# Optimization experiments

Measured on AMD Instinct MI355X. Metric: run time of the kernel, lower is better.

The kernel has to match this reference:

```python
import jax, jax.numpy as jnp
import numpy as np
from jax import lax

C_IN, C_OUT, LEVEL = 64, 128, 4
SOFTMAX_SCALE = 10.0
ESCAPE_NAN = 1e-4


def conv3(x, w, b):
    y = lax.conv_general_dilated(x, w, (1, 1), [(1, 1), (1, 1)],
                                 dimension_numbers=('NCHW', 'OIHW', 'NCHW'))
    return y + b[None, :, None, None]


def conv1(x, w, b):  # 1x1 conv, w: [O, I]
    return jnp.einsum('oi,bihw->bohw', w, x) + b[None, :, None, None]


def prelu(x, a):
    return jnp.where(x >= 0, x, a * x)


def resblock(x, w1, b1, w2, b2):  # EDSR ResBlock, res_scale=1
    return x + conv3(jax.nn.relu(conv3(x, w1, b1)), w2, b2)


def patches9(x):
    # 3x3 'same' (zero-pad 1) patches: [B,C,H,W] -> [B,C,3,3,H*W], (C,kh,kw) order like torch unfold
    B, C, H, W = x.shape
    xp = jnp.pad(x, ((0, 0), (0, 0), (1, 1), (1, 1)))
    p = jnp.stack([xp[:, :, i:i + H, j:j + W] for i in range(3) for j in range(3)], axis=2)
    return p.reshape(B, C, 3, 3, H * W)


def pyramid_attention(x, mbw, mbb, mba, mw, mb_, ma, aw, ab, aa):
    B, C, H, W = x.shape
    C2 = C // 2
    scales = [1.0 - i / 10 for i in range(LEVEL)]
    match_base = prelu(conv1(x, mbw, mbb), mba)            # [B,C2,H,W]
    xp = patches9(match_base).reshape(B, C2 * 9, H * W)    # query patches (same-padded input to conv2d)
    w_all, rw_all = [], []
    for s in scales:
        if s != 1.0:
            Hs, Ws = int(H * s), int(W * s)
            ref = jax.image.resize(x, (B, C, Hs, Ws), method='bilinear')
        else:
            ref = x
        base = prelu(conv1(ref, aw, ab), aa)               # conv_assembly: [B,C,Hs,Ws]
        rw_all.append(jnp.transpose(patches9(base), (0, 4, 1, 2, 3)))   # [B,L,C,3,3]
        refm = prelu(conv1(ref, mw, mb_), ma)              # conv_match:    [B,C2,Hs,Ws]
        w_all.append(jnp.transpose(patches9(refm), (0, 4, 1, 2, 3)))    # [B,L,C2,3,3]
    wi = jnp.concatenate(w_all, axis=1)                    # [B,Lt,C2,3,3]
    rw = jnp.concatenate(rw_all, axis=1)                   # [B,Lt,C,3,3]
    Lt = wi.shape[1]
    norm = jnp.maximum(jnp.sqrt(jnp.sum(wi * wi, axis=(2, 3, 4), keepdims=True)), ESCAPE_NAN)
    wn = (wi / norm).reshape(B, Lt, C2 * 9)
    # conv2d-as-correlation: scores[b,l,p] = <patch_p(match_base_b), wn[b,l]>
    scores = jnp.einsum('blk,bkp->blp', wn, xp)            # [B,Lt,H*W]
    att = jax.nn.softmax(scores * SOFTMAX_SCALE, axis=1).reshape(B, Lt, H, W)

    def tconv(y, rw_b):  # conv_transpose2d(stride=1, padding=1) == conv with swapped+flipped kernel
        wk = jnp.flip(jnp.transpose(rw_b, (1, 0, 2, 3)), axis=(2, 3))  # [C,Lt,3,3]
        return lax.conv_general_dilated(y[None], wk, (1, 1), [(1, 1), (1, 1)],
                                        dimension_numbers=('NCHW', 'OIHW', 'NCHW'))[0]

    out = jax.vmap(tconv)(att, rw) / 4.0
    return out + x  # res_scale = 1


def reference(x, bb0_w, bb0_b, bb0_a, rb1_w1, rb1_b1, rb1_w2, rb1_b2,
              pamb_w, pamb_b, pamb_a, pam_w, pam_b, pam_a, paa_w, paa_b, paa_a,
              rb2_w1, rb2_b1, rb2_w2, rb2_b2):
    h = lax.reduce_window(x, -jnp.inf, lax.max, (1, 1, 2, 2), (1, 1, 2, 2), 'VALID')  # MaxPool2d(2)
    h = prelu(conv3(h, bb0_w, bb0_b), bb0_a)               # BasicBlock in->out
    h = resblock(h, rb1_w1, rb1_b1, rb1_w2, rb1_b2)
    h = pyramid_attention(h, pamb_w, pamb_b, pamb_a, pam_w, pam_b, pam_a, paa_w, paa_b, paa_a)
    h = resblock(h, rb2_w1, rb2_b1, rb2_w2, rb2_b2)
    return h


def setup_inputs() -> dict:
    key = jax.random.key(0)
    ks = jax.random.split(key, 20)
    B, H, W = 2, 128, 128
    Ci, Co = C_IN, C_OUT
    C2 = Co // 2

    def n(k, shape, s=0.05):
        return jax.random.normal(k, shape, jnp.float32) * s

    a = jnp.asarray(0.25, jnp.float32)  # PReLU default init
    return {
        'x': jax.random.normal(ks[0], (B, Ci, H, W), jnp.float32),
        'bb0_w': n(ks[1], (Co, Ci, 3, 3)), 'bb0_b': n(ks[2], (Co,)), 'bb0_a': a,
        'rb1_w1': n(ks[3], (Co, Co, 3, 3)), 'rb1_b1': n(ks[4], (Co,)),
        'rb1_w2': n(ks[5], (Co, Co, 3, 3)), 'rb1_b2': n(ks[6], (Co,)),
        'pamb_w': n(ks[7], (C2, Co)), 'pamb_b': n(ks[8], (C2,)), 'pamb_a': a,
        'pam_w': n(ks[9], (C2, Co)), 'pam_b': n(ks[10], (C2,)), 'pam_a': a,
        'paa_w': n(ks[11], (Co, Co)), 'paa_b': n(ks[12], (Co,)), 'paa_a': a,
        'rb2_w1': n(ks[13], (Co, Co, 3, 3)), 'rb2_b1': n(ks[14], (Co,)),
        'rb2_w2': n(ks[15], (Co, Co, 3, 3)), 'rb2_b2': n(ks[16], (Co,)),
    }
```

## Files before the change

### kernel.cpp

```cpp
#include <hip/hip_runtime.h>

typedef unsigned short u16;
typedef __attribute__((ext_vector_type(8))) __bf16 bf16x8;
typedef __attribute__((ext_vector_type(8))) unsigned short ushort8;
typedef __attribute__((ext_vector_type(4))) float f32x4;

__device__ __forceinline__ float bf2f(u16 u) { return __uint_as_float(((unsigned)u) << 16); }
__device__ __forceinline__ u16 f2bf(float f) {
    unsigned x = __float_as_uint(f);
    x += 0x7fffu + ((x >> 16) & 1u);
    return (u16)(x >> 16);
}

#define LP 13824

__global__ __launch_bounds__(256) void d7_gemm(
    const u16* __restrict__ A, const u16* __restrict__ B,
    int N, int K, int kLen, int mTiles, int S,
    long aBS, long bBS,
    const float* __restrict__ bias, const float* __restrict__ alpha, int act,
    const float* __restrict__ resid, long residBS,
    float* __restrict__ outF, long oFBS,
    u16* __restrict__ outB, long oBBS,
    float* __restrict__ outP, long pMN)
{
    __shared__ u16 As[128 * 40];
    __shared__ u16 Bs[128 * 40];

    const int tid = threadIdx.x;
    const int wv = tid >> 6, lane = tid & 63;
    const int wm = wv >> 1, wn = wv & 1;
    const int bn = blockIdx.x;
    const int bm = blockIdx.y % mTiles;
    const int ks = blockIdx.y / mTiles;
    const int z  = blockIdx.z;
    const int kStart = ks * kLen;

    const int srow = tid >> 1;
    const int soff = (tid & 1) * 16;
    const u16* gA = A + z * aBS + (size_t)(bm * 128 + srow) * K + kStart + soff;
    const u16* gB = B + z * bBS + (size_t)(bn * 128 + srow) * K + kStart + soff;
    u16* lA = &As[srow * 40 + soff];
    u16* lB = &Bs[srow * 40 + soff];

    f32x4 acc[4][4] = {};

    for (int k0 = 0; k0 < kLen; k0 += 32) {
        __syncthreads();
        ((uint4*)lA)[0] = ((const uint4*)gA)[0];
        ((uint4*)lA)[1] = ((const uint4*)gA)[1];
        ((uint4*)lB)[0] = ((const uint4*)gB)[0];
        ((uint4*)lB)[1] = ((const uint4*)gB)[1];
        gA += 32; gB += 32;
        __syncthreads();

        bf16x8 a[4], b[4];
        #pragma unroll
        for (int mt = 0; mt < 4; ++mt)
            a[mt] = *reinterpret_cast<const bf16x8*>(&As[(wm * 64 + mt * 16 + (lane & 15)) * 40 + (lane >> 4) * 8]);
        #pragma unroll
        for (int nt = 0; nt < 4; ++nt)
            b[nt] = *reinterpret_cast<const bf16x8*>(&Bs[(wn * 64 + nt * 16 + (lane & 15)) * 40 + (lane >> 4) * 8]);
        #pragma unroll
        for (int mt = 0; mt < 4; ++mt)
            #pragma unroll
            for (int nt = 0; nt < 4; ++nt)
                acc[mt][nt] = __builtin_amdgcn_mfma_f32_16x16x32_bf16(a[mt], b[nt], acc[mt][nt], 0, 0, 0);
    }

    if (outP) {
        float* pp = outP + ((size_t)z * S + ks) * pMN;
        #pragma unroll
        for (int mt = 0; mt < 4; ++mt) {
            const int mg = bm * 128 + wm * 64 + mt * 16 + ((lane >> 4) << 2);
            #pragma unroll
            for (int nt = 0; nt < 4; ++nt) {
                const int ng = bn * 128 + wn * 64 + nt * 16 + (lane & 15);
                #pragma unroll
                for (int r = 0; r < 4; ++r)
                    pp[(size_t)(mg + r) * N + ng] = acc[mt][nt][r];
            }
        }
        return;
    }

    const float aval = (act == 1) ? alpha[0] : 0.0f;
    #pragma unroll
    for (int mt = 0; mt < 4; ++mt) {
        const int mg = bm * 128 + wm * 64 + mt * 16 + ((lane >> 4) << 2);
        float bv[4] = {0.f, 0.f, 0.f, 0.f};
        if (bias) {
            #pragma unroll
            for (int r = 0; r < 4; ++r) bv[r] = bias[mg + r];
        }
        #pragma unroll
        for (int nt = 0; nt < 4; ++nt) {
            const int ng = bn * 128 + wn * 64 + nt * 16 + (lane & 15);
            #pragma unroll
            for (int r = 0; r < 4; ++r) {
                float t = acc[mt][nt][r] + bv[r];
                if (act == 1) t = (t >= 0.f) ? t : aval * t;
                else if (act == 2) t = fmaxf(t, 0.f);
                if (resid) t += resid[z * residBS + (size_t)(mg + r) * N + ng];
                if (outF) outF[z * oFBS + (size_t)(mg + r) * N + ng] = t;
                if (outB) outB[z * oBBS + (size_t)(mg + r) * N + ng] = f2bf(t);
            }
        }
    }
}

__global__ __launch_bounds__(256) void d7_epi(
    const float* __restrict__ parts, int S, long sStride, long bStride,
    const float* __restrict__ bias, const float* __restrict__ alpha, int act,
    const float* __restrict__ resid, long residBS, float scale,
    float* __restrict__ out, long outBS, int total)
{
    int i = blockIdx.x * 256 + threadIdx.x;
    if (i >= total) return;
    int b = blockIdx.z;
    const float* p = parts + b * bStride + i;
    float s = 0.f;
    for (int t = 0; t < S; ++t) s += p[(size_t)t * sStride];
    s *= scale;
    if (bias) s += bias[i >> 12];
    if (act == 1) { float a = alpha[0]; s = (s >= 0.f) ? s : a * s; }
    else if (act == 2) s = fmaxf(s, 0.f);
    if (resid) s += resid[b * residBS + i];
    out[b * outBS + i] = s;
}

__global__ __launch_bounds__(256) void d7_cast(const float* __restrict__ src, u16* __restrict__ dst, int n) {
    int i = blockIdx.x * 256 + threadIdx.x;
    if (i < n) dst[i] = f2bf(src[i]);
}

__global__ __launch_bounds__(256) void d7_maxpool(const float* __restrict__ x, float* __restrict__ out) {
    int p = blockIdx.x * 256 + threadIdx.x;
    int c = blockIdx.y, b = blockIdx.z;
    int oh = p >> 6, ow = p & 63;
    const float* ip = x + ((size_t)b * 64 + c) * 16384;
    float v0 = ip[(2 * oh) * 128 + 2 * ow];
    float v1 = ip[(2 * oh) * 128 + 2 * ow + 1];
    float v2 = ip[(2 * oh + 1) * 128 + 2 * ow];
    float v3 = ip[(2 * oh + 1) * 128 + 2 * ow + 1];
    out[((size_t)b * 64 + c) * 4096 + p] = fmaxf(fmaxf(v0, v1), fmaxf(v2, v3));
}

__global__ __launch_bounds__(256) void d7_im2col(const float* __restrict__ img, u16* __restrict__ patT,
                                                 int Cin, long inBS, long outBS) {
    int K = Cin * 9;
    int k = blockIdx.x * 256 + threadIdx.x;
    if (k >= K) return;
    int p = blockIdx.y, b = blockIdx.z;
    int c = k / 9, k9 = k - c * 9;
    int h = p >> 6, w = p & 63;
    int y = h + k9 / 3 - 1, x = w + (k9 % 3) - 1;
    const float* ip = img + b * inBS;
    float v = (y >= 0 && y < 64 && x >= 0 && x < 64) ? ip[(size_t)c * 4096 + y * 64 + x] : 0.f;
    patT[b * outBS + (size_t)p * K + k] = f2bf(v);
}

__global__ __launch_bounds__(256) void d7_c1T(
    const float* __restrict__ in, long inBS, const float* __restrict__ Wm,
    const float* __restrict__ bias, const float* __restrict__ alpha,
    int P, u16* __restrict__ out, long outBS, int HS, int Wp, int off)
{
    int p = blockIdx.x * 256 + threadIdx.x;
    if (p >= P) return;
    int co = blockIdx.y, b = blockIdx.z;
    const float* ip = in + b * inBS;
    float acc = bias[co];
    for (int ci = 0; ci < 128; ++ci) acc += Wm[co * 128 + ci] * ip[(size_t)ci * P + p];
    float a = alpha[0];
    acc = (acc >= 0.f) ? acc : a * acc;
    int hs = p / HS, ws = p - hs * HS;
    int lp = off + (hs + 1) * Wp + ws + 1;
    out[b * outBS + (size_t)lp * 64 + co] = f2bf(acc);
}

__global__ __launch_bounds__(256) void d7_c1N(
    const float* __restrict__ in, long inBS, const float* __restrict__ Wm,
    const float* __restrict__ bias, const float* __restrict__ alpha,
    int P, u16* __restrict__ out, long outBS, int HS, int Wp, int off)
{
    int p = blockIdx.x * 256 + threadIdx.x;
    if (p >= P) return;
    int co = blockIdx.y, b = blockIdx.z;
    const float* ip = in + b * inBS;
    float acc = bias[co];
    for (int ci = 0; ci < 128; ++ci) acc += Wm[co * 128 + ci] * ip[(size_t)ci * P + p];
    float a = alpha[0];
    acc = (acc >= 0.f) ? acc : a * acc;
    int hs = p / HS, ws = p - hs * HS;
    int lp = off + (hs + 1) * Wp + ws + 1;
    out[b * outBS + (size_t)co * LP + lp] = f2bf(acc);
}

template <int OS>
__device__ __forceinline__ void d7_taps(int o, int& i0, float w3[3]) {
    const float inv = 64.0f / OS;
    float s = (o + 0.5f) * inv - 0.5f;
    i0 = (int)ceilf(s - inv);
    float wsum = 0.f;
    #pragma unroll
    for (int t = 0; t < 3; ++t) {
        int y = i0 + t;
        float wt = 1.0f - fabsf((float)y - s) / inv;
        wt = (wt > 0.f && y >= 0 && y < 64) ? wt : 0.f;
        w3[t] = wt; wsum += wt;
    }
    float r = 1.0f / wsum;
    w3[0] *= r; w3[1] *= r; w3[2] *= r;
}

template <int OS>
__global__ __launch_bounds__(256) void d7_resize(const float* __restrict__ in, float* __restrict__ out, long out_bs) {
    int p = blockIdx.x * 256 + threadIdx.x;
    if (p >= OS * OS) return;
    int c = blockIdx.y, b = blockIdx.z;
    int oh = p / OS, ow = p - oh * OS;
    const float* img = in + ((size_t)b * 128 + c) * 4096;
    int y0, x0; float wy[3], wx[3];
    d7_taps<OS>(oh, y0, wy);
    d7_taps<OS>(ow, x0, wx);
    float sum = 0.f;
    #pragma unroll
    for (int iy = 0; iy < 3; ++iy) {
        if (wy[iy] <= 0.f) continue;
        float rs = 0.f;
        #pragma unroll
        for (int ix = 0; ix < 3; ++ix) {
            if (wx[ix] <= 0.f) continue;
            rs += wx[ix] * img[(y0 + iy) * 64 + (x0 + ix)];
        }
        sum += wy[iy] * rs;
    }
    out[(size_t)b * out_bs + (size_t)c * OS * OS + p] = sum;
}

__device__ __forceinline__ int d7_scaleW(int l) {
    return (l < 4752) ? 72 : (l < 8528) ? 64 : (l < 11496) ? 56 : 48;
}

__global__ __launch_bounds__(256) void d7_s2(const u16* __restrict__ refmT, float* __restrict__ s2) {
    int l = blockIdx.x * 256 + threadIdx.x;
    if (l >= LP) return;
    int zb = blockIdx.z;
    const u16* r = refmT + (size_t)zb * LP * 64 + (size_t)l * 64;
    float s = 0.f;
    #pragma unroll
    for (int c8 = 0; c8 < 8; ++c8) {
        ushort8 v = *reinterpret_cast<const ushort8*>(r + c8 * 8);
        #pragma unroll
        for (int i = 0; i < 8; ++i) { float f = bf2f(v[i]); s += f * f; }
    }
    s2[zb * LP + l] = s;
}

__global__ __launch_bounds__(256) void d7_rnormk(const float* __restrict__ s2, float* __restrict__ rnorm) {
    int l = blockIdx.x * 256 + threadIdx.x;
    if (l >= LP) return;
    int zb = blockIdx.z;
    int off, W, HS;
    if (l < 4752)       { off = 0;     W = 72; HS = 64; }
    else if (l < 8528)  { off = 4752;  W = 64; HS = 57; }
    else if (l < 11496) { off = 8528;  W = 56; HS = 51; }
    else                { off = 11496; W = 48; HS = 44; }
    int li = l - off, y = li / W, x = li - y * W;
    float v = 0.f;
    if (y >= 1 && y <= HS && x >= 1 && x <= HS) {
        const float* s = s2 + zb * LP;
        float a = 0.f;
        #pragma unroll
        for (int dy = -1; dy <= 1; ++dy)
            #pragma unroll
            for (int dx = -1; dx <= 1; ++dx)
                a += s[l + dy * W + dx];
        v = 1.f / fmaxf(sqrtf(a), 1e-4f);
    }
    rnorm[zb * LP + l] = v;
}

__global__ __launch_bounds__(256) void d7_st1(const u16* __restrict__ in, u16* __restrict__ out,
                                              const float* __restrict__ rnorm) {
    int vg = blockIdx.x * 256 + threadIdx.x;
    if (vg >= LP / 8) return;
    int l8 = vg << 3;
    int p = blockIdx.y;
    int h = p >> 6, w = p & 63;
    int W = d7_scaleW(l8);
    float acc[8] = {0.f, 0.f, 0.f, 0.f, 0.f, 0.f, 0.f, 0.f};
    #pragma unroll
    for (int a = -1; a <= 1; ++a) {
        int ph = h + a;
        if ((unsigned)ph >= 64u) continue;
        #pragma unroll
        for (int b = -1; b <= 1; ++b) {
            int pw = w + b;
            if ((unsigned)pw >= 64u) continue;
            const u16* rp = in + (size_t)(p + a * 64 + b) * LP + l8 + a * W;
            ushort8 v = *reinterpret_cast<const ushort8*>(rp);
            if (b == 0) {
                #pragma unroll
                for (int i = 0; i < 8; ++i) acc[i] += bf2f(v[i]);
            } else if (b == -1) {
                acc[0] += bf2f(rp[-1]);
                #pragma unroll
                for (int i = 1; i < 8; ++i) acc[i] += bf2f(v[i - 1]);
            } else {
                acc[7] += bf2f(rp[8]);
                #pragma unroll
                for (int i = 0; i < 7; ++i) acc[i] += bf2f(v[i + 1]);
            }
        }
    }
    const float4 rn0 = *reinterpret_cast<const float4*>(rnorm + l8);
    const float4 rn1 = *reinterpret_cast<const float4*>(rnorm + l8 + 4);
    float rn[8] = {rn0.x, rn0.y, rn0.z, rn0.w, rn1.x, rn1.y, rn1.z, rn1.w};
    ushort8 res;
    #pragma unroll
    for (int i = 0; i < 8; ++i)
        res[i] = f2bf((rn[i] != 0.f) ? acc[i] * rn[i] : -1e4f);
    *reinterpret_cast<ushort8*>(out + (size_t)p * LP + l8) = res;
}

__global__ __launch_bounds__(256) void d7_stats(const u16* __restrict__ sc, float2* __restrict__ stat) {
    int p = blockIdx.x, tid = threadIdx.x, wv = tid >> 6, lane = tid & 63;
    const u16* row = sc + (size_t)p * LP;
    float m = -3e38f;
    #pragma unroll
    for (int it = 0; it < 7; ++it) {
        int vg = tid + it * 256;
        if (vg < LP / 8) {
            ushort8 v = *reinterpret_cast<const ushort8*>(row + vg * 8);
            #pragma unroll
            for (int i = 0; i < 8; ++i) m = fmaxf(m, bf2f(v[i]));
        }
    }
    #pragma unroll
    for (int o = 1; o < 64; o <<= 1) m = fmaxf(m, __shfl_xor(m, o));
    __shared__ float red[4];
    if (lane == 0) red[wv] = m;
    __syncthreads();
    m = fmaxf(fmaxf(red[0], red[1]), fmaxf(red[2], red[3]));
    __syncthreads();
    float s = 0.f;
    #pragma unroll
    for (int it = 0; it < 7; ++it) {
        int vg = tid + it * 256;
        if (vg < LP / 8) {
            ushort8 v = *reinterpret_cast<const ushort8*>(row + vg * 8);
            #pragma unroll
            for (int i = 0; i < 8; ++i) s += __expf((bf2f(v[i]) - m) * 10.f);
        }
    }
    #pragma unroll
    for (int o = 1; o < 64; o <<= 1) s += __shfl_xor(s, o);
    if (lane == 0) red[wv] = s;
    __syncthreads();
    if (tid == 0) {
        float Z = red[0] + red[1] + red[2] + red[3];
        stat[p] = make_float2(m, 1.0f / Z);
    }
}

__global__ __launch_bounds__(256) void d7_st2(const u16* __restrict__ in,
                                              const float2* __restrict__ stat,
                                              const float* __restrict__ rnorm,
                                              u16* __restrict__ out) {
    int vg = blockIdx.x * 256 + threadIdx.x;
    if (vg >= LP / 8) return;
    int l8 = vg << 3;
    int p = blockIdx.y;
    int h = p >> 6, w = p & 63;
    int W = d7_scaleW(l8);
    float acc[8] = {0.f, 0.f, 0.f, 0.f, 0.f, 0.f, 0.f, 0.f};
    #pragma unroll
    for (int a = -1; a <= 1; ++a) {
        int ph = h + a;
        if ((unsigned)ph >= 64u) continue;
        #pragma unroll
        for (int b = -1; b <= 1; ++b) {
            int pw = w + b;
            if ((unsigned)pw >= 64u) continue;
            int r = p + a * 64 + b;
            float2 st = stat[r];
            const u16* rp = in + (size_t)r * LP + l8 + a * W;
            ushort8 v = *reinterpret_cast<const ushort8*>(rp);
            if (b == 0) {
                #pragma unroll
                for (int i = 0; i < 8; ++i) acc[i] += __expf((bf2f(v[i]) - st.x) * 10.f) * st.y;
            } else if (b == -1) {
                acc[0] += __expf((bf2f(rp[-1]) - st.x) * 10.f) * st.y;
                #pragma unroll
                for (int i = 1; i < 8; ++i) acc[i] += __expf((bf2f(v[i - 1]) - st.x) * 10.f) * st.y;
            } else {
                acc[7] += __expf((bf2f(rp[8]) - st.x) * 10.f) * st.y;
                #pragma unroll
                for (int i = 0; i < 7; ++i) acc[i] += __expf((bf2f(v[i + 1]) - st.x) * 10.f) * st.y;
            }
        }
    }
    const float4 rn0 = *reinterpret_cast<const float4*>(rnorm + l8);
    const float4 rn1 = *reinterpret_cast<const float4*>(rnorm + l8 + 4);
    float rn[8] = {rn0.x, rn0.y, rn0.z, rn0.w, rn1.x, rn1.y, rn1.z, rn1.w};
    ushort8 res;
    #pragma unroll
    for (int i = 0; i < 8; ++i)
        res[i] = f2bf((rn[i] != 0.f) ? acc[i] : 0.f);
    *reinterpret_cast<ushort8*>(out + (size_t)p * LP + l8) = res;
}

extern "C" void kernel_launch(void* const* d_in, const int* in_sizes, int n_in,
                              void* d_out, int out_size, void* d_ws, size_t ws_size,
                              hipStream_t stream) {
    const float* x      = (const float*)d_in[0];
    const float* bb0_w  = (const float*)d_in[1];
    const float* bb0_b  = (const float*)d_in[2];
    const float* bb0_a  = (const float*)d_in[3];
    const float* rb1_w1 = (const float*)d_in[4];
    const float* rb1_b1 = (const float*)d_in[5];
    const float* rb1_w2 = (const float*)d_in[6];
    const float* rb1_b2 = (const float*)d_in[7];
    const float* pamb_w = (const float*)d_in[8];
    const float* pamb_b = (const float*)d_in[9];
    const float* pamb_a = (const float*)d_in[10];
    const float* pam_w  = (const float*)d_in[11];
    const float* pam_b  = (const float*)d_in[12];
    const float* pam_a  = (const float*)d_in[13];
    const float* paa_w  = (const float*)d_in[14];
    const float* paa_b  = (const float*)d_in[15];
    const float* paa_a  = (const float*)d_in[16];
    const float* rb2_w1 = (const float*)d_in[17];
    const float* rb2_b1 = (const float*)d_in[18];
    const float* rb2_w2 = (const float*)d_in[19];
    const float* rb2_b2 = (const float*)d_in[20];
    float* out = (float*)d_out;
    (void)in_sizes; (void)n_in; (void)out_size; (void)ws_size;

    char* wp = (char*)d_ws;
    auto alloc = [&](size_t nbytes) { void* p = wp; wp += (nbytes + 255) & ~(size_t)255; return p; };
    const size_t BIG = 4096ull * LP * 2;
    char* big1r  = (char*)alloc(BIG + 1024);
    char* big2r  = (char*)alloc(BIG + 1024);
    float* h0f   = (float*)alloc(2ull * 64 * 4096 * 4);
    float* h1f   = (float*)alloc(2ull * 128 * 4096 * 4);
    float* h2f   = (float*)alloc(2ull * 128 * 4096 * 4);
    float* paf   = (float*)alloc(2ull * 128 * 4096 * 4);
    float* tbuf  = (float*)alloc(2ull * 128 * 4096 * 4);
    float* refb  = (float*)alloc(2ull * 128 * 7786 * 4);
    u16* mbT     = (u16*)alloc(2ull * 4096 * 64 * 2);
    u16* refmT   = (u16*)alloc(2ull * LP * 64 * 2);
    u16* baseA   = (u16*)alloc(2ull * 128 * LP * 2);
    float* s2b   = (float*)alloc(2ull * LP * 4);
    float* rnorm = (float*)alloc(2ull * LP * 4);
    float2* stat = (float2*)alloc(4096ull * 8);
    u16* A0      = (u16*)alloc(73728ull * 2);
    u16* A1      = (u16*)alloc(147456ull * 2);
    u16* A2      = (u16*)alloc(147456ull * 2);
    u16* A3      = (u16*)alloc(147456ull * 2);
    u16* A4      = (u16*)alloc(147456ull * 2);

    u16* patT    = (u16*)big1r;
    u16* S0T     = (u16*)(big1r + 512);
    u16* gT      = (u16*)(big1r + 512);
    u16* scT     = (u16*)(big2r + 512);
    float* parts = (float*)big2r;

    const long h2bs = 128L * 4096;
    const long pMN = 128L * 4096;
    const long refbs = 128L * 7786;
    const long mbTbs = 4096L * 64, rmTbs = (long)LP * 64, baBS = 128L * LP;

    auto conv = [&](const float* src, const u16* W, int Cin, const float* bias,
                    const float* alpha, int act, const float* resid, float* dst) {
        int K = Cin * 9;
        d7_im2col<<<dim3((K + 255) / 256, 4096, 2), 256, 0, stream>>>(src, patT, Cin, (long)Cin * 4096, 4096L * K);
        d7_gemm<<<dim3(32, 6, 2), 256, 0, stream>>>(W, patT, 4096, K, K / 6, 1, 6,
            0, 4096L * K, nullptr, nullptr, 0, nullptr, 0,
            nullptr, 0, nullptr, 0, parts, pMN);
        d7_epi<<<dim3(2048, 1, 2), 256, 0, stream>>>(parts, 6, pMN, 6 * pMN,
            bias, alpha, act, resid, h2bs, 1.0f, dst, h2bs, (int)pMN);
    };

    d7_cast<<<dim3(288), 256, 0, stream>>>(bb0_w, A0, 73728);
    d7_cast<<<dim3(576), 256, 0, stream>>>(rb1_w1, A1, 147456);
    d7_cast<<<dim3(576), 256, 0, stream>>>(rb1_w2, A2, 147456);
    d7_cast<<<dim3(576), 256, 0, stream>>>(rb2_w1, A3, 147456);
    d7_cast<<<dim3(576), 256, 0, stream>>>(rb2_w2, A4, 147456);

    d7_maxpool<<<dim3(16, 64, 2), 256, 0, stream>>>(x, h0f);
    conv(h0f, A0, 64, bb0_b, bb0_a, 1, nullptr, h1f);
    conv(h1f, A1, 128, rb1_b1, nullptr, 2, nullptr, tbuf);
    conv(tbuf, A2, 128, rb1_b2, nullptr, 0, h1f, h2f);

    d7_resize<57><<<dim3(13, 128, 2), 256, 0, stream>>>(h2f, refb, refbs);
    d7_resize<51><<<dim3(11, 128, 2), 256, 0, stream>>>(h2f, refb + 3249L * 128, refbs);
    d7_resize<44><<<dim3(8, 128, 2), 256, 0, stream>>>(h2f, refb + 5850L * 128, refbs);

    hipMemsetAsync(refmT, 0, 2ull * LP * 64 * 2, stream);
    hipMemsetAsync(baseA, 0, 2ull * 128 * LP * 2, stream);
    d7_c1T<<<dim3(16, 64, 2), 256, 0, stream>>>(h2f, h2bs, pamb_w, pamb_b, pamb_a, 4096, mbT, mbTbs, 64, 64, -65);
    d7_c1T<<<dim3(16, 64, 2), 256, 0, stream>>>(h2f, h2bs, pam_w, pam_b, pam_a, 4096, refmT, rmTbs, 64, 72, 0);
    d7_c1T<<<dim3(13, 64, 2), 256, 0, stream>>>(refb, refbs, pam_w, pam_b, pam_a, 3249, refmT, rmTbs, 57, 64, 4752);
    d7_c1T<<<dim3(11, 64, 2), 256, 0, stream>>>(refb + 3249L * 128, refbs, pam_w, pam_b, pam_a, 2601, refmT, rmTbs, 51, 56, 8528);
    d7_c1T<<<dim3(8, 64, 2), 256, 0, stream>>>(refb + 5850L * 128, refbs, pam_w, pam_b, pam_a, 1936, refmT, rmTbs, 44, 48, 11496);
    d7_c1N<<<dim3(16, 128, 2), 256, 0, stream>>>(h2f, h2bs, paa_w, paa_b, paa_a, 4096, baseA, baBS, 64, 72, 0);
    d7_c1N<<<dim3(13, 128, 2), 256, 0, stream>>>(refb, refbs, paa_w, paa_b, paa_a, 3249, baseA, baBS, 57, 64, 4752);
    d7_c1N<<<dim3(11, 128, 2), 256, 0, stream>>>(refb + 3249L * 128, refbs, paa_w, paa_b, paa_a, 2601, baseA, baBS, 51, 56, 8528);
    d7_c1N<<<dim3(8, 128, 2), 256, 0, stream>>>(refb + 5850L * 128, refbs, paa_w, paa_b, paa_a, 1936, baseA, baBS, 44, 48, 11496);

    d7_s2<<<dim3(54, 1, 2), 256, 0, stream>>>(refmT, s2b);
    d7_rnormk<<<dim3(54, 1, 2), 256, 0, stream>>>(s2b, rnorm);

    for (int b = 0; b < 2; ++b) {
        d7_gemm<<<dim3(LP / 128, 32, 1), 256, 0, stream>>>(mbT + b * mbTbs, refmT + b * rmTbs,
            LP, 64, 64, 32, 1, 0, 0, nullptr, nullptr, 0, nullptr, 0,
            nullptr, 0, S0T, 0, nullptr, 0);
        d7_st1<<<dim3(7, 4096), 256, 0, stream>>>(S0T, scT, rnorm + b * LP);
        d7_stats<<<dim3(4096), 256, 0, stream>>>(scT, stat);
        d7_st2<<<dim3(7, 4096), 256, 0, stream>>>(scT, stat, rnorm + b * LP, gT);
        d7_gemm<<<dim3(32, 12, 1), 256, 0, stream>>>(baseA + b * baBS, gT,
            4096, LP, LP / 12, 1, 12, 0, 0, nullptr, nullptr, 0, nullptr, 0,
            nullptr, 0, nullptr, 0, parts, pMN);
        d7_epi<<<dim3(2048, 1, 1), 256, 0, stream>>>(parts, 12, pMN, 0,
            nullptr, nullptr, 0, h2f + b * h2bs, 0, 0.25f, paf + b * h2bs, 0, (int)pMN);
    }

    conv(paf, A3, 128, rb2_b1, nullptr, 2, nullptr, tbuf);
    conv(tbuf, A4, 128, rb2_b2, nullptr, 0, paf, out);
}
```

Before: 1.087 ms.

## Move attention 1x1 convs onto MFMA GEMM and store softmax scores in fp16

The scalar 1x1 convolution kernels that built the match and assembly features are replaced by two batched bf16 MFMA GEMMs with concatenated weights and per-row PReLU. Their inputs are produced by tiled transposes, and their outputs are scattered into the padded layouts by small copy kernels. The score GEMM now emits a transposed packed store, and the softmax scale of 10 is folded into the inverse norm. Intermediate scores are kept as fp16 instead of bf16, which gives more mantissa but less range, and the extra launches plus transpose and scatter passes add memory traffic.

```diff
diff --git a/kernel.cpp b/kernel.cpp
--- a/kernel.cpp
+++ b/kernel.cpp
@@ -10,6 +10,12 @@
     unsigned x = __float_as_uint(f);
     x += 0x7fffu + ((x >> 16) & 1u);
     return (u16)(x >> 16);
+}
+__device__ __forceinline__ u16 f2h16(float f) {
+    _Float16 h = (_Float16)f; u16 r; __builtin_memcpy(&r, &h, 2); return r;
+}
+__device__ __forceinline__ float h162f(u16 u) {
+    _Float16 h; __builtin_memcpy(&h, &u, 2); return (float)h;
 }
 
 #define LP 13824
@@ -22,6 +28,7 @@
     const float* __restrict__ resid, long residBS,
     float* __restrict__ outF, long oFBS,
     u16* __restrict__ outB, long oBBS,
+    u16* __restrict__ outT, int ldT, long oTBS,
     float* __restrict__ outP, long pMN)
 {
     __shared__ u16 As[128 * 40];
@@ -84,26 +91,46 @@
         return;
     }
 
-    const float aval = (act == 1) ? alpha[0] : 0.0f;
+    const float avalS = (act == 1) ? alpha[0] : 0.0f;
     #pragma unroll
     for (int mt = 0; mt < 4; ++mt) {
         const int mg = bm * 128 + wm * 64 + mt * 16 + ((lane >> 4) << 2);
-        float bv[4] = {0.f, 0.f, 0.f, 0.f};
+        float bv[4] = {0.f, 0.f, 0.f, 0.f}, av[4];
         if (bias) {
             #pragma unroll
             for (int r = 0; r < 4; ++r) bv[r] = bias[mg + r];
+        }
+        if (act == 3) {
+            #pragma unroll
+            for (int r = 0; r < 4; ++r) av[r] = alpha[mg + r];
         }
         #pragma unroll
         for (int nt = 0; nt < 4; ++nt) {
             const int ng = bn * 128 + wn * 64 + nt * 16 + (lane & 15);
+            float v[4];
             #pragma unroll
             for (int r = 0; r < 4; ++r) {
                 float t = acc[mt][nt][r] + bv[r];
-                if (act == 1) t = (t >= 0.f) ? t : aval * t;
+                if (act == 1) t = (t >= 0.f) ? t : avalS * t;
                 else if (act == 2) t = fmaxf(t, 0.f);
+                else if (act == 3) t = (t >= 0.f) ? t : av[r] * t;
                 if (resid) t += resid[z * residBS + (size_t)(mg + r) * N + ng];
-                if (outF) outF[z * oFBS + (size_t)(mg + r) * N + ng] = t;
-                if (outB) outB[z * oBBS + (size_t)(mg + r) * N + ng] = f2bf(t);
+                v[r] = t;
+            }
+            if (outF) {
+                #pragma unroll
+                for (int r = 0; r < 4; ++r) outF[z * oFBS + (size_t)(mg + r) * N + ng] = v[r];
+            }
+            if (outB) {
+                #pragma unroll
+                for (int r = 0; r < 4; ++r) outB[z * oBBS + (size_t)(mg + r) * N + ng] = f2bf(v[r]);
+            }
+            if (outT) {
+                unsigned long long pk = (unsigned long long)f2bf(v[0])
+                    | ((unsigned long long)f2bf(v[1]) << 16)
+                    | ((unsigned long long)f2bf(v[2]) << 32)
+                    | ((unsigned long long)f2bf(v[3]) << 48);
+                *reinterpret_cast<unsigned long long*>(outT + z * oTBS + (size_t)ng * ldT + mg) = pk;
             }
         }
     }
@@ -134,6 +161,31 @@
     if (i < n) dst[i] = f2bf(src[i]);
 }
 
+__global__ __launch_bounds__(256) void d7_wbuild(
+    const float* __restrict__ pamb_w, const float* __restrict__ pam_w, const float* __restrict__ paa_w,
+    const float* __restrict__ pamb_b, const float* __restrict__ pam_b, const float* __restrict__ paa_b,
+    const float* __restrict__ pamb_a, const float* __restrict__ pam_a, const float* __restrict__ paa_a,
+    u16* __restrict__ W1, u16* __restrict__ W2,
+    float* __restrict__ b1, float* __restrict__ a1,
+    float* __restrict__ b2, float* __restrict__ a2)
+{
+    int i = blockIdx.x * 256 + threadIdx.x;
+    if (i < 256 * 128) {
+        int r = i >> 7, c = i & 127;
+        float w1 = (r < 64) ? pamb_w[r * 128 + c] : (r < 128) ? pam_w[(r - 64) * 128 + c] : paa_w[(r - 128) * 128 + c];
+        W1[i] = f2bf(w1);
+        float w2 = (r < 64) ? pam_w[r * 128 + c] : (r < 192) ? paa_w[(r - 64) * 128 + c] : 0.f;
+        W2[i] = f2bf(w2);
+    }
+    if (i < 256) {
+        int r = i;
+        b1[r] = (r < 64) ? pamb_b[r] : (r < 128) ? pam_b[r - 64] : paa_b[r - 128];
+        a1[r] = (r < 64) ? pamb_a[0] : (r < 128) ? pam_a[0] : paa_a[0];
+        b2[r] = (r < 64) ? pam_b[r] : (r < 192) ? paa_b[r - 64] : 0.f;
+        a2[r] = (r < 64) ? pam_a[0] : (r < 192) ? paa_a[0] : 0.f;
+    }
+}
+
 __global__ __launch_bounds__(256) void d7_maxpool(const float* __restrict__ x, float* __restrict__ out) {
     int p = blockIdx.x * 256 + threadIdx.x;
     int c = blockIdx.y, b = blockIdx.z;
@@ -160,40 +212,49 @@
     patT[b * outBS + (size_t)p * K + k] = f2bf(v);
 }
 
-__global__ __launch_bounds__(256) void d7_c1T(
-    const float* __restrict__ in, long inBS, const float* __restrict__ Wm,
-    const float* __restrict__ bias, const float* __restrict__ alpha,
-    int P, u16* __restrict__ out, long outBS, int HS, int Wp, int off)
-{
+__global__ __launch_bounds__(256) void d7_t32(const float* __restrict__ in, long inBS, int P,
+                                              u16* __restrict__ out, long outBS) {
+    __shared__ float tile[32][33];
+    int p0 = blockIdx.x * 32, c0 = blockIdx.y * 32, b = blockIdx.z;
+    int tx = threadIdx.x & 31, ty = threadIdx.x >> 5;
+    const float* ip = in + b * inBS;
+    #pragma unroll
+    for (int i = 0; i < 32; i += 8) {
+        int c = c0 + ty + i, p = p0 + tx;
+        tile[ty + i][tx] = (p < P) ? ip[(size_t)c * P + p] : 0.f;
+    }
+    __syncthreads();
+    u16* op = out + b * outBS;
+    #pragma unroll
+    for (int i = 0; i < 32; i += 8) {
+        int p = p0 + ty + i, c = c0 + tx;
+        if (p < P) op[(size_t)p * 128 + c] = f2bf(tile[tx][ty + i]);
+    }
+}
+
+__global__ __launch_bounds__(256) void d7_scK(const u16* __restrict__ cT, long cBS, int ldC, int colBase,
+                                              int pOff, int P, int HS, int Wp, int off,
+                                              u16* __restrict__ dst, long dBS) {
+    int t = blockIdx.x * 256 + threadIdx.x;
+    int p = t >> 3, cg = t & 7;
+    if (p >= P) return;
+    int b = blockIdx.z;
+    ushort8 v = *reinterpret_cast<const ushort8*>(cT + b * cBS + (size_t)(pOff + p) * ldC + colBase + cg * 8);
+    int h = p / HS, w = p - h * HS;
+    int lp = off + (h + 1) * Wp + w + 1;
+    *reinterpret_cast<ushort8*>(dst + b * dBS + (size_t)lp * 64 + cg * 8) = v;
+}
+
+__global__ __launch_bounds__(256) void d7_scR(const u16* __restrict__ cO, long cBS, int ldC, int rowBase,
+                                              int pOff, int P, int HS, int Wp, int off,
+                                              u16* __restrict__ dst, long dBS) {
     int p = blockIdx.x * 256 + threadIdx.x;
     if (p >= P) return;
     int co = blockIdx.y, b = blockIdx.z;
-    const float* ip = in + b * inBS;
-    float acc = bias[co];
-    for (int ci = 0; ci < 128; ++ci) acc += Wm[co * 128 + ci] * ip[(size_t)ci * P + p];
-    float a = alpha[0];
-    acc = (acc >= 0.f) ? acc : a * acc;
-    int hs = p / HS, ws = p - hs * HS;
-    int lp = off + (hs + 1) * Wp + ws + 1;
-    out[b * outBS + (size_t)lp * 64 + co] = f2bf(acc);
-}
-
-__global__ __launch_bounds__(256) void d7_c1N(
-    const float* __restrict__ in, long inBS, const float* __restrict__ Wm,
-    const float* __restrict__ bias, const float* __restrict__ alpha,
-    int P, u16* __restrict__ out, long outBS, int HS, int Wp, int off)
-{
-    int p = blockIdx.x * 256 + threadIdx.x;
-    if (p >= P) return;
-    int co = blockIdx.y, b = blockIdx.z;
-    const float* ip = in + b * inBS;
-    float acc = bias[co];
-    for (int ci = 0; ci < 128; ++ci) acc += Wm[co * 128 + ci] * ip[(size_t)ci * P + p];
-    float a = alpha[0];
-    acc = (acc >= 0.f) ? acc : a * acc;
-    int hs = p / HS, ws = p - hs * HS;
-    int lp = off + (hs + 1) * Wp + ws + 1;
-    out[b * outBS + (size_t)co * LP + lp] = f2bf(acc);
+    u16 v = cO[b * cBS + (size_t)(rowBase + co) * ldC + pOff + p];
+    int h = p / HS, w = p - h * HS;
+    int lp = off + (h + 1) * Wp + w + 1;
+    dst[b * dBS + (size_t)co * LP + lp] = v;
 }
 
 template <int OS>
@@ -276,7 +337,7 @@
             #pragma unroll
             for (int dx = -1; dx <= 1; ++dx)
                 a += s[l + dy * W + dx];
-        v = 1.f / fmaxf(sqrtf(a), 1e-4f);
+        v = 10.f / fmaxf(sqrtf(a), 1e-4f);
     }
     rnorm[zb * LP + l] = v;
 }
@@ -320,7 +381,7 @@
     ushort8 res;
     #pragma unroll
     for (int i = 0; i < 8; ++i)
-        res[i] = f2bf((rn[i] != 0.f) ? acc[i] * rn[i] : -1e4f);
+        res[i] = f2h16((rn[i] != 0.f) ? acc[i] * rn[i] : -1e4f);
     *reinterpret_cast<ushort8*>(out + (size_t)p * LP + l8) = res;
 }
 
@@ -334,7 +395,7 @@
         if (vg < LP / 8) {
             ushort8 v = *reinterpret_cast<const ushort8*>(row + vg * 8);
             #pragma unroll
-            for (int i = 0; i < 8; ++i) m = fmaxf(m, bf2f(v[i]));
+            for (int i = 0; i < 8; ++i) m = fmaxf(m, h162f(v[i]));
         }
     }
     #pragma unroll
@@ -351,7 +412,7 @@
         if (vg < LP / 8) {
             ushort8 v = *reinterpret_cast<const ushort8*>(row + vg * 8);
             #pragma unroll
-            for (int i = 0; i < 8; ++i) s += __expf((bf2f(v[i]) - m) * 10.f);
+            for (int i = 0; i < 8; ++i) s += __expf(h162f(v[i]) - m);
         }
     }
     #pragma unroll
@@ -389,15 +450,15 @@
             ushort8 v = *reinterpret_cast<const ushort8*>(rp);
             if (b == 0) {
                 #pragma unroll
-                for (int i = 0; i < 8; ++i) acc[i] += __expf((bf2f(v[i]) - st.x) * 10.f) * st.y;
+                for (int i = 0; i < 8; ++i) acc[i] += __expf(h162f(v[i]) - st.x) * st.y;
             } else if (b == -1) {
-                acc[0] += __expf((bf2f(rp[-1]) - st.x) * 10.f) * st.y;
-                #pragma unroll
-                for (int i = 1; i < 8; ++i) acc[i] += __expf((bf2f(v[i - 1]) - st.x) * 10.f) * st.y;
+                acc[0] += __expf(h162f(rp[-1]) - st.x) * st.y;
+                #pragma unroll
+                for (int i = 1; i < 8; ++i) acc[i] += __expf(h162f(v[i - 1]) - st.x) * st.y;
             } else {
-                acc[7] += __expf((bf2f(rp[8]) - st.x) * 10.f) * st.y;
-                #pragma unroll
-                for (int i = 0; i < 7; ++i) acc[i] += __expf((bf2f(v[i + 1]) - st.x) * 10.f) * st.y;
+                acc[7] += __expf(h162f(rp[8]) - st.x) * st.y;
+                #pragma unroll
+                for (int i = 0; i < 7; ++i) acc[i] += __expf(h162f(v[i + 1]) - st.x) * st.y;
             }
         }
     }
@@ -448,29 +509,43 @@
     float* h2f   = (float*)alloc(2ull * 128 * 4096 * 4);
     float* paf   = (float*)alloc(2ull * 128 * 4096 * 4);
     float* tbuf  = (float*)alloc(2ull * 128 * 4096 * 4);
-    float* refb  = (float*)alloc(2ull * 128 * 7786 * 4);
     u16* mbT     = (u16*)alloc(2ull * 4096 * 64 * 2);
     u16* refmT   = (u16*)alloc(2ull * LP * 64 * 2);
     u16* baseA   = (u16*)alloc(2ull * 128 * LP * 2);
     float* s2b   = (float*)alloc(2ull * LP * 4);
     float* rnorm = (float*)alloc(2ull * LP * 4);
     float2* stat = (float2*)alloc(4096ull * 8);
+    u16* W1      = (u16*)alloc(256ull * 128 * 2);
+    u16* W2      = (u16*)alloc(256ull * 128 * 2);
+    float* b1v   = (float*)alloc(256 * 4);
+    float* a1v   = (float*)alloc(256 * 4);
+    float* b2v   = (float*)alloc(256 * 4);
+    float* a2v   = (float*)alloc(256 * 4);
     u16* A0      = (u16*)alloc(73728ull * 2);
     u16* A1      = (u16*)alloc(147456ull * 2);
     u16* A2      = (u16*)alloc(147456ull * 2);
     u16* A3      = (u16*)alloc(147456ull * 2);
     u16* A4      = (u16*)alloc(147456ull * 2);
-
     u16* patT    = (u16*)big1r;
+    u16* h2T     = (u16*)big1r;
+    u16* refbT   = (u16*)(big1r + (4ull << 20));
     u16* S0T     = (u16*)(big1r + 512);
     u16* gT      = (u16*)(big1r + 512);
+    float* parts = (float*)big2r;
+    u16* cT1     = (u16*)big2r;
+    u16* cOut1   = (u16*)(big2r + (4ull << 20));
+    u16* cT2     = (u16*)(big2r + (8ull << 20));
+    u16* cOut2   = (u16*)(big2r + (16ull << 20));
+    float* refb  = (float*)(big2r + (26ull << 20));
     u16* scT     = (u16*)(big2r + 512);
-    float* parts = (float*)big2r;
 
     const long h2bs = 128L * 4096;
     const long pMN = 128L * 4096;
     const long refbs = 128L * 7786;
     const long mbTbs = 4096L * 64, rmTbs = (long)LP * 64, baBS = 128L * LP;
+    const long cT1bs = 4096L * 256, cO1bs = 256L * 4096;
+    const long cT2bs = 7808L * 256, cO2bs = 256L * 7808;
+    const long rbTbs = 7808L * 128;
 
     auto conv = [&](const float* src, const u16* W, int Cin, const float* bias,
                     const float* alpha, int act, const float* resid, float* dst) {
@@ -478,7 +553,7 @@
         d7_im2col<<<dim3((K + 255) / 256, 4096, 2), 256, 0, stream>>>(src, patT, Cin, (long)Cin * 4096, 4096L * K);
         d7_gemm<<<dim3(32, 6, 2), 256, 0, stream>>>(W, patT, 4096, K, K / 6, 1, 6,
             0, 4096L * K, nullptr, nullptr, 0, nullptr, 0,
-            nullptr, 0, nullptr, 0, parts, pMN);
+            nullptr, 0, nullptr, 0, nullptr, 0, 0, parts, pMN);
         d7_epi<<<dim3(2048, 1, 2), 256, 0, stream>>>(parts, 6, pMN, 6 * pMN,
             bias, alpha, act, resid, h2bs, 1.0f, dst, h2bs, (int)pMN);
     };
@@ -488,6 +563,8 @@
     d7_cast<<<dim3(576), 256, 0, stream>>>(rb1_w2, A2, 147456);
     d7_cast<<<dim3(576), 256, 0, stream>>>(rb2_w1, A3, 147456);
     d7_cast<<<dim3(576), 256, 0, stream>>>(rb2_w2, A4, 147456);
+    d7_wbuild<<<dim3(128), 256, 0, stream>>>(pamb_w, pam_w, paa_w, pamb_b, pam_b, paa_b,
+                                             pamb_a, pam_a, paa_a, W1, W2, b1v, a1v, b2v, a2v);
 
     d7_maxpool<<<dim3(16, 64, 2), 256, 0, stream>>>(x, h0f);
     conv(h0f, A0, 64, bb0_b, bb0_a, 1, nullptr, h1f);
@@ -498,31 +575,44 @@
     d7_resize<51><<<dim3(11, 128, 2), 256, 0, stream>>>(h2f, refb + 3249L * 128, refbs);
     d7_resize<44><<<dim3(8, 128, 2), 256, 0, stream>>>(h2f, refb + 5850L * 128, refbs);
 
+    hipMemsetAsync(refbT, 0, 2ull * rbTbs * 2, stream);
+    d7_t32<<<dim3(128, 4, 2), 256, 0, stream>>>(h2f, h2bs, 4096, h2T, 4096L * 128);
+    d7_t32<<<dim3(102, 4, 2), 256, 0, stream>>>(refb, refbs, 3249, refbT, rbTbs);
+    d7_t32<<<dim3(82, 4, 2), 256, 0, stream>>>(refb + 3249L * 128, refbs, 2601, refbT + 3249L * 128, rbTbs);
+    d7_t32<<<dim3(61, 4, 2), 256, 0, stream>>>(refb + 5850L * 128, refbs, 1936, refbT + 5850L * 128, rbTbs);
+
+    d7_gemm<<<dim3(32, 2, 2), 256, 0, stream>>>(W1, h2T, 4096, 128, 128, 2, 1,
+        0, 4096L * 128, b1v, a1v, 3, nullptr, 0,
+        nullptr, 0, cOut1, cO1bs, cT1, 256, cT1bs, nullptr, 0);
+    d7_gemm<<<dim3(61, 2, 2), 256, 0, stream>>>(W2, refbT, 7808, 128, 128, 2, 1,
+        0, rbTbs, b2v, a2v, 3, nullptr, 0,
+        nullptr, 0, cOut2, cO2bs, cT2, 256, cT2bs, nullptr, 0);
+
     hipMemsetAsync(refmT, 0, 2ull * LP * 64 * 2, stream);
     hipMemsetAsync(baseA, 0, 2ull * 128 * LP * 2, stream);
-    d7_c1T<<<dim3(16, 64, 2), 256, 0, stream>>>(h2f, h2bs, pamb_w, pamb_b, pamb_a, 4096, mbT, mbTbs, 64, 64, -65);
-    d7_c1T<<<dim3(16, 64, 2), 256, 0, stream>>>(h2f, h2bs, pam_w, pam_b, pam_a, 4096, refmT, rmTbs, 64, 72, 0);
-    d7_c1T<<<dim3(13, 64, 2), 256, 0, stream>>>(refb, refbs, pam_w, pam_b, pam_a, 3249, refmT, rmTbs, 57, 64, 4752);
-    d7_c1T<<<dim3(11, 64, 2), 256, 0, stream>>>(refb + 3249L * 128, refbs, pam_w, pam_b, pam_a, 2601, refmT, rmTbs, 51, 56, 8528);
-    d7_c1T<<<dim3(8, 64, 2), 256, 0, stream>>>(refb + 5850L * 128, refbs, pam_w, pam_b, pam_a, 1936, refmT, rmTbs, 44, 48, 11496);
-    d7_c1N<<<dim3(16, 128, 2), 256, 0, stream>>>(h2f, h2bs, paa_w, paa_b, paa_a, 4096, baseA, baBS, 64, 72, 0);
-    d7_c1N<<<dim3(13, 128, 2), 256, 0, stream>>>(refb, refbs, paa_w, paa_b, paa_a, 3249, baseA, baBS, 57, 64, 4752);
-    d7_c1N<<<dim3(11, 128, 2), 256, 0, stream>>>(refb + 3249L * 128, refbs, paa_w, paa_b, paa_a, 2601, baseA, baBS, 51, 56, 8528);
-    d7_c1N<<<dim3(8, 128, 2), 256, 0, stream>>>(refb + 5850L * 128, refbs, paa_w, paa_b, paa_a, 1936, baseA, baBS, 44, 48, 11496);
+    d7_scK<<<dim3(128, 1, 2), 256, 0, stream>>>(cT1, cT1bs, 256, 0, 0, 4096, 64, 64, -65, mbT, mbTbs);
+    d7_scK<<<dim3(128, 1, 2), 256, 0, stream>>>(cT1, cT1bs, 256, 64, 0, 4096, 64, 72, 0, refmT, rmTbs);
+    d7_scK<<<dim3(102, 1, 2), 256, 0, stream>>>(cT2, cT2bs, 256, 0, 0, 3249, 57, 64, 4752, refmT, rmTbs);
+    d7_scK<<<dim3(82, 1, 2), 256, 0, stream>>>(cT2, cT2bs, 256, 0, 3249, 2601, 51, 56, 8528, refmT, rmTbs);
+    d7_scK<<<dim3(61, 1, 2), 256, 0, stream>>>(cT2, cT2bs, 256, 0, 5850, 1936, 44, 48, 11496, refmT, rmTbs);
+    d7_scR<<<dim3(16, 128, 2), 256, 0, stream>>>(cOut1, cO1bs, 4096, 128, 0, 4096, 64, 72, 0, baseA, baBS);
+    d7_scR<<<dim3(13, 128, 2), 256, 0, stream>>>(cOut2, cO2bs, 7808, 64, 0, 3249, 57, 64, 4752, baseA, baBS);
+    d7_scR<<<dim3(11, 128, 2), 256, 0, stream>>>(cOut2, cO2bs, 7808, 64, 3249, 2601, 51, 56, 8528, baseA, baBS);
+    d7_scR<<<dim3(8, 128, 2), 256, 0, stream>>>(cOut2, cO2bs, 7808, 64, 5850, 1936, 44, 48, 11496, baseA, baBS);
 
     d7_s2<<<dim3(54, 1, 2), 256, 0, stream>>>(refmT, s2b);
     d7_rnormk<<<dim3(54, 1, 2), 256, 0, stream>>>(s2b, rnorm);
 
     for (int b = 0; b < 2; ++b) {
-        d7_gemm<<<dim3(LP / 128, 32, 1), 256, 0, stream>>>(mbT + b * mbTbs, refmT + b * rmTbs,
-            LP, 64, 64, 32, 1, 0, 0, nullptr, nullptr, 0, nullptr, 0,
-            nullptr, 0, S0T, 0, nullptr, 0);
+        d7_gemm<<<dim3(32, 108, 1), 256, 0, stream>>>(refmT + b * rmTbs, mbT + b * mbTbs,
+            4096, 64, 64, 108, 1, 0, 0, nullptr, nullptr, 0, nullptr, 0,
+            nullptr, 0, nullptr, 0, S0T, LP, 0, nullptr, 0);
         d7_st1<<<dim3(7, 4096), 256, 0, stream>>>(S0T, scT, rnorm + b * LP);
         d7_stats<<<dim3(4096), 256, 0, stream>>>(scT, stat);
         d7_st2<<<dim3(7, 4096), 256, 0, stream>>>(scT, stat, rnorm + b * LP, gT);
         d7_gemm<<<dim3(32, 12, 1), 256, 0, stream>>>(baseA + b * baBS, gT,
             4096, LP, LP / 12, 1, 12, 0, 0, nullptr, nullptr, 0, nullptr, 0,
-            nullptr, 0, nullptr, 0, parts, pMN);
+            nullptr, 0, nullptr, 0, nullptr, 0, 0, parts, pMN);
         d7_epi<<<dim3(2048, 1, 1), 256, 0, stream>>>(parts, 12, pMN, 0,
             nullptr, nullptr, 0, h2f + b * h2bs, 0, 0.25f, paf + b * h2bs, 0, (int)pMN);
     }
```

After: 1.005 ms. -7.5%, faster.
